# Performance work log

Measured on AMD Instinct MI355X. Metric: run time of the kernel, lower is better.

The kernel has to match this reference:

```python
import jax, jax.numpy as jnp
import numpy as np

B, S, D = 8, 2048, 512


def setup_inputs() -> dict:
    key = jax.random.key(0)
    ks = jax.random.split(key, 11)
    scale = 1.0 / np.sqrt(D)
    inp = {"x": jax.random.normal(ks[0], (B, S, D), dtype=jnp.float32)}
    names = ["q", "k", "v", "g", "o"]
    for i, n in enumerate(names):
        inp[f"W{n}"] = jax.random.normal(ks[1 + 2 * i], (D, D), dtype=jnp.float32) * scale
        inp[f"b{n}"] = jax.random.normal(ks[2 + 2 * i], (D,), dtype=jnp.float32) * 0.01
    return inp


def reference(x, Wq, bq, Wk, bk, Wv, bv, Wg, bg, Wo, bo):
    # Projections (torch nn.Linear: x @ W.T + b)
    Q = x @ Wq.T + bq            # (B,S,D)
    K = x @ Wk.T + bk
    V = x @ Wv.T + bv
    gamma = jax.nn.sigmoid(x @ Wg.T + bg)

    # Recurrent linear-attention scan over time.
    # State St: (B,D,D); update: St = gamma_t[:, :, None] * St + k_t ⊗ v_t
    # (decay broadcasts along the key/row dimension, matching
    #  gamma_i.transpose(1,2) * S in the torch code)
    def step(St, qkvg):
        q_t, k_t, v_t, g_t = qkvg           # each (B,D)
        St = g_t[:, :, None] * St + k_t[:, :, None] * v_t[:, None, :]
        out_t = jnp.einsum('bd,bde->be', q_t, St)  # q_i @ S
        return St, out_t

    S0 = jnp.zeros((B, D, D), dtype=x.dtype)
    # time-major inputs for scan: (S,B,D)
    seq = (Q.transpose(1, 0, 2), K.transpose(1, 0, 2),
           V.transpose(1, 0, 2), gamma.transpose(1, 0, 2))
    _, outs = jax.lax.scan(step, S0, seq)   # outs: (S,B,D)
    O = outs.transpose(1, 0, 2)             # (B,S,D)
    return O @ Wo.T + bo
```

## Files before the change

### kernel.cpp

```cpp
#include <hip/hip_runtime.h>
#include <hip/hip_bf16.h>
#include <stdint.h>


#define B_ 8
#define S_ 2048
#define D_ 512
#define M_ (B_ * S_)
#define NSUB 64
#define SUBL 32
#define NSUP 8
#define SUPL 256

typedef __bf16 bf16x8 __attribute__((ext_vector_type(8)));
typedef float f32x4 __attribute__((ext_vector_type(4)));

__device__ __forceinline__ float bflo(uint32_t u){ return __uint_as_float(u<<16); }
__device__ __forceinline__ float bfhi(uint32_t u){ return __uint_as_float(u&0xffff0000u); }
__device__ __forceinline__ uint16_t f2bf(float f){
    uint32_t u = __float_as_uint(f);
    return (uint16_t)((u + 0x7fffu + ((u>>16)&1u)) >> 16);
}
__device__ __forceinline__ uint32_t pack2bf(float a, float b){
    return (uint32_t)f2bf(a) | ((uint32_t)f2bf(b)<<16);
}
__device__ __forceinline__ void gload16(const void* g, void* l){
    __builtin_amdgcn_global_load_lds(
        (const __attribute__((address_space(1))) uint32_t*)g,
        (__attribute__((address_space(3))) uint32_t*)l, 16, 0, 0);
}

__global__ __launch_bounds__(256) void conv_x(const float* __restrict__ in,
                                              uint16_t* __restrict__ out){
    const size_t i = ((size_t)blockIdx.x*256 + threadIdx.x)*8;
    float4 a = *(const float4*)&in[i];
    float4 b = *(const float4*)&in[i+4];
    uint4 o; o.x=pack2bf(a.x,a.y); o.y=pack2bf(a.z,a.w); o.z=pack2bf(b.x,b.y); o.w=pack2bf(b.z,b.w);
    *(uint4*)&out[i] = o;
}
__global__ __launch_bounds__(256) void conv_w(const float* w0, const float* w1, const float* w2,
                                              const float* w3, const float* w4,
                                              uint16_t* __restrict__ out){
    const float* ws[5] = {w0,w1,w2,w3,w4};
    const float* in = ws[blockIdx.y];
    uint16_t* o = out + (size_t)blockIdx.y*D_*D_;
    const size_t i = ((size_t)blockIdx.x*256 + threadIdx.x)*8;
    float4 a = *(const float4*)&in[i];
    float4 b = *(const float4*)&in[i+4];
    uint4 u; u.x=pack2bf(a.x,a.y); u.y=pack2bf(a.z,a.w); u.z=pack2bf(b.x,b.y); u.w=pack2bf(b.z,b.w);
    *(uint4*)&o[i] = u;
}

__global__ __launch_bounds__(256) void proj4(const uint16_t* __restrict__ A,
                                             const uint16_t* __restrict__ Wb,
                                             const float* __restrict__ bq_,
                                             const float* __restrict__ bk_,
                                             const float* __restrict__ bv_,
                                             const float* __restrict__ bg_,
                                             uint16_t* __restrict__ Qb,
                                             uint16_t* __restrict__ Kb,
                                             uint16_t* __restrict__ VT,
                                             float* __restrict__ Gf)
{
    __shared__ __attribute__((aligned(16))) uint16_t As[128*64];
    __shared__ __attribute__((aligned(16))) uint16_t Bs[128*64];
    const int tid = threadIdx.x, wave = tid>>6, lane = tid&63;
    const int m0 = blockIdx.x*128, n0 = blockIdx.y*128;
    const int wr = (wave>>1)*64, wc = (wave&1)*64;
    const int fr = lane&15, fq = lane>>4;
    f32x4 acc[4][4] = {};

    for (int k0 = 0; k0 < D_; k0 += 64) {
        __syncthreads();
#pragma unroll
        for (int i = 0; i < 4; ++i) {
            const int c = i*256 + tid;
            const int row = c>>3, kc = (c&7)*8;
            const int ldsb = (i*256 + wave*64)*8;
            gload16(&A [(size_t)(m0+row)*D_ + k0 + kc], &As[ldsb]);
            gload16(&Wb[(size_t)(n0+row)*D_ + k0 + kc], &Bs[ldsb]);
        }
        __syncthreads();
#pragma unroll
        for (int kk = 0; kk < 64; kk += 32) {
            bf16x8 af[4], bf[4];
#pragma unroll
            for (int m = 0; m < 4; ++m) af[m] = *(const bf16x8*)&As[(wr+m*16+fr)*64 + kk + fq*8];
#pragma unroll
            for (int n = 0; n < 4; ++n) bf[n] = *(const bf16x8*)&Bs[(wc+n*16+fr)*64 + kk + fq*8];
#pragma unroll
            for (int m = 0; m < 4; ++m)
#pragma unroll
                for (int n = 0; n < 4; ++n)
                    acc[m][n] = __builtin_amdgcn_mfma_f32_16x16x32_bf16(af[m], bf[n], acc[m][n], 0,0,0);
        }
    }
    const int sect = blockIdx.y >> 2;
    const float* bias = (sect==0) ? bq_ : (sect==1) ? bk_ : (sect==2) ? bv_ : bg_;
#pragma unroll
    for (int n = 0; n < 4; ++n) {
        const int coll = (n0 & 511) + wc + n*16 + fr;
        const float bv = bias[coll];
        if (sect == 2) {
#pragma unroll
            for (int m = 0; m < 4; ++m) {
                const int rg = m0 + wr + m*16 + fq*4;
                const int bb = rg >> 11, t = rg & 2047;
                uint2 pk;
                pk.x = pack2bf(acc[m][n][0]+bv, acc[m][n][1]+bv);
                pk.y = pack2bf(acc[m][n][2]+bv, acc[m][n][3]+bv);
                *(uint2*)&VT[((size_t)bb*D_ + coll)*S_ + t] = pk;
            }
        } else if (sect == 3) {
#pragma unroll
            for (int m = 0; m < 4; ++m)
#pragma unroll
                for (int q = 0; q < 4; ++q) {
                    const int row = m0 + wr + m*16 + fq*4 + q;
                    Gf[(size_t)row*D_ + coll] = 1.f/(1.f+expf(-(acc[m][n][q]+bv)));
                }
        } else {
            uint16_t* dst = sect ? Kb : Qb;
#pragma unroll
            for (int m = 0; m < 4; ++m)
#pragma unroll
                for (int q = 0; q < 4; ++q) {
                    const int row = m0 + wr + m*16 + fq*4 + q;
                    dst[(size_t)row*D_ + coll] = f2bf(acc[m][n][q]+bv);
                }
        }
    }
}

__global__ __launch_bounds__(256) void mfma_gemm(const uint16_t* __restrict__ A,
                                                 const uint16_t* __restrict__ Wt,
                                                 const float* __restrict__ bias,
                                                 float* __restrict__ out)
{
    __shared__ __attribute__((aligned(16))) uint16_t As[128*64];
    __shared__ __attribute__((aligned(16))) uint16_t Bs[128*64];
    const int tid = threadIdx.x, wave = tid>>6, lane = tid&63;
    const int m0 = blockIdx.x*128, n0 = blockIdx.y*128;
    const int wr = (wave>>1)*64, wc = (wave&1)*64;
    const int fr = lane&15, fq = lane>>4;
    f32x4 acc[4][4] = {};

    for (int k0 = 0; k0 < D_; k0 += 64) {
        __syncthreads();
#pragma unroll
        for (int i = 0; i < 4; ++i) {
            const int c = i*256 + tid;
            const int row = c>>3, kc = (c&7)*8;
            const int ldsb = (i*256 + wave*64)*8;
            gload16(&A [(size_t)(m0+row)*D_ + k0 + kc], &As[ldsb]);
            gload16(&Wt[(size_t)(n0+row)*D_ + k0 + kc], &Bs[ldsb]);
        }
        __syncthreads();
#pragma unroll
        for (int kk = 0; kk < 64; kk += 32) {
            bf16x8 af[4], bf[4];
#pragma unroll
            for (int m = 0; m < 4; ++m) af[m] = *(const bf16x8*)&As[(wr+m*16+fr)*64 + kk + fq*8];
#pragma unroll
            for (int n = 0; n < 4; ++n) bf[n] = *(const bf16x8*)&Bs[(wc+n*16+fr)*64 + kk + fq*8];
#pragma unroll
            for (int m = 0; m < 4; ++m)
#pragma unroll
                for (int n = 0; n < 4; ++n)
                    acc[m][n] = __builtin_amdgcn_mfma_f32_16x16x32_bf16(af[m], bf[n], acc[m][n], 0,0,0);
        }
    }
#pragma unroll
    for (int n = 0; n < 4; ++n) {
        const int col = n0 + wc + n*16 + fr;
        const float bv = bias[col];
#pragma unroll
        for (int m = 0; m < 4; ++m)
#pragma unroll
            for (int q = 0; q < 4; ++q) {
                const int row = m0 + wr + m*16 + fq*4 + q;
                out[(size_t)row*D_ + col] = acc[m][n][q] + bv;
            }
    }
}

__global__ __launch_bounds__(256) void prep(const float* __restrict__ Gf,
                                            uint16_t* __restrict__ Qb,
                                            uint16_t* __restrict__ Kb,
                                            uint16_t* __restrict__ KT,
                                            float* __restrict__ T)
{
    const int sub = blockIdx.x, b = blockIdx.y;
    const int tid = threadIdx.x;
    const int dk0 = tid*2;
    const size_t rowbase = ((size_t)b*S_ + sub*SUBL)*D_;
    const float*    gp = Gf + rowbase + dk0;
    uint16_t*       qp = Qb + rowbase + dk0;
    uint16_t*       kp = Kb + rowbase + dk0;

    float mu0 = 1.f, mu1 = 1.f;
    uint32_t ksave[SUBL];
#pragma unroll
    for (int t = 0; t < SUBL; ++t) {
        const float2   g  = *(const float2*)(gp + (size_t)t*D_);
        const uint32_t qu = *(const uint32_t*)(qp + (size_t)t*D_);
        const uint32_t ku = *(const uint32_t*)(kp + (size_t)t*D_);
        mu0 = fmaxf(mu0*g.x, 1e-30f);
        mu1 = fmaxf(mu1*g.y, 1e-30f);
        const float r0 = __builtin_amdgcn_rcpf(mu0);
        const float r1 = __builtin_amdgcn_rcpf(mu1);
        *(uint32_t*)(qp + (size_t)t*D_) = pack2bf(bflo(qu)*mu0, bfhi(qu)*mu1);
        const uint32_t kw = pack2bf(bflo(ku)*r0, bfhi(ku)*r1);
        *(uint32_t*)(kp + (size_t)t*D_) = kw;
        ksave[t] = kw;
    }
    T[((size_t)b*NSUB + sub)*D_ + dk0]     = mu0;
    T[((size_t)b*NSUB + sub)*D_ + dk0 + 1] = mu1;

    uint16_t* d0 = &KT[((size_t)b*D_ + dk0)*S_ + sub*SUBL];
    uint16_t* d1 = d0 + S_;
#pragma unroll
    for (int q4 = 0; q4 < 4; ++q4) {
        uint4 lo, hi;
        lo.x = (ksave[q4*8+0]&0xffffu) | (ksave[q4*8+1]<<16);
        lo.y = (ksave[q4*8+2]&0xffffu) | (ksave[q4*8+3]<<16);
        lo.z = (ksave[q4*8+4]&0xffffu) | (ksave[q4*8+5]<<16);
        lo.w = (ksave[q4*8+6]&0xffffu) | (ksave[q4*8+7]<<16);
        hi.x = (ksave[q4*8+0]>>16) | (ksave[q4*8+1]&0xffff0000u);
        hi.y = (ksave[q4*8+2]>>16) | (ksave[q4*8+3]&0xffff0000u);
        hi.z = (ksave[q4*8+4]>>16) | (ksave[q4*8+5]&0xffff0000u);
        hi.w = (ksave[q4*8+6]>>16) | (ksave[q4*8+7]&0xffff0000u);
        *(uint4*)&d0[q4*8] = lo;
        *(uint4*)&d1[q4*8] = hi;
    }
}

__global__ __launch_bounds__(512) void tables(const float* __restrict__ T,
                                              float* __restrict__ Pre,
                                              float* __restrict__ Suf,
                                              float* __restrict__ Lam)
{
    const int b = blockIdx.x, dk = threadIdx.x;
    for (int sp = 0; sp < NSUP; ++sp) {
        float run = 1.f;
#pragma unroll
        for (int m = 0; m < 8; ++m) {
            Pre[((size_t)b*NSUB + sp*8+m)*D_ + dk] = run;
            run *= T[((size_t)b*NSUB + sp*8+m)*D_ + dk];
        }
        Lam[((size_t)b*NSUP + sp)*D_ + dk] = run;
        float rs = 1.f;
#pragma unroll
        for (int m = 7; m >= 0; --m) {
            rs *= T[((size_t)b*NSUB + sp*8+m)*D_ + dk];
            Suf[((size_t)b*NSUB + sp*8+m)*D_ + dk] = rs;
        }
    }
}

__device__ __forceinline__ int swz(int r, int c){ return r*D_ + (c ^ ((r&7)<<3)); }

__global__ __launch_bounds__(256) void pairsA(const uint16_t* __restrict__ Qt,
                                              const uint16_t* __restrict__ Kh,
                                              const float* __restrict__ T,
                                              uint16_t* __restrict__ P)
{
    __shared__ __attribute__((aligned(16))) uint16_t qs[SUBL*D_];
    __shared__ __attribute__((aligned(16))) uint16_t ks[SUBL*D_];
    __shared__ float D_lds[D_];
    const int bx = blockIdx.x, sp = blockIdx.y, b = blockIdx.z;
    const int tid = threadIdx.x, wave = tid>>6, lane = tid&63;
    const int fr = lane&15, fq = lane>>4;
    const int mq = wave>>1, nq = wave&1;
    const int dkA = tid*2, dkB = tid*2+1;

    for (int ii = 0; ii < 2; ++ii) {
        const int i = ii ? 7-bx : bx;
        const size_t qrow = (size_t)b*S_ + sp*SUPL + i*SUBL;
        const size_t prow = ((size_t)(b*NSUP + sp)*SUPL + i*SUBL);

#pragma unroll
        for (int z = 0; z < 8; ++z) {
            int ch = z*256 + tid, r = ch>>6, c = (ch&63)*8;
            *(uint4*)&qs[swz(r,c)] = *(const uint4*)&Qt[(qrow + r)*D_ + c];
            *(uint4*)&ks[swz(r,c)] = *(const uint4*)&Kh[(qrow + r)*D_ + c];
        }
        float d0 = 1.f, d1 = 1.f;

        for (int j = i; j >= 0; --j) {
            if (j < i) {
                d0 *= T[((size_t)b*NSUB + sp*8 + j)*D_ + dkA];
                d1 *= T[((size_t)b*NSUB + sp*8 + j)*D_ + dkB];
                D_lds[dkA] = d0; D_lds[dkB] = d1;
                __syncthreads();
#pragma unroll
                for (int z = 0; z < 8; ++z) {
                    int ch = z*256 + tid, r = ch>>6, c = (ch&63)*8;
                    uint4 u = *(const uint4*)&Kh[((size_t)b*S_ + sp*SUPL + j*SUBL + r)*D_ + c];
                    uint4 o;
                    o.x = pack2bf(bflo(u.x)*D_lds[c+0], bfhi(u.x)*D_lds[c+1]);
                    o.y = pack2bf(bflo(u.y)*D_lds[c+2], bfhi(u.y)*D_lds[c+3]);
                    o.z = pack2bf(bflo(u.z)*D_lds[c+4], bfhi(u.z)*D_lds[c+5]);
                    o.w = pack2bf(bflo(u.w)*D_lds[c+6], bfhi(u.w)*D_lds[c+7]);
                    *(uint4*)&ks[swz(r,c)] = o;
                }
            }
            __syncthreads();
            f32x4 a0 = {}, a1 = {}, a2 = {}, a3 = {};
#pragma unroll
            for (int kk = 0; kk < 512; kk += 128) {
                bf16x8 q0 = *(const bf16x8*)&qs[swz(mq*16+fr, kk      + fq*8)];
                bf16x8 k0 = *(const bf16x8*)&ks[swz(nq*16+fr, kk      + fq*8)];
                bf16x8 q1 = *(const bf16x8*)&qs[swz(mq*16+fr, kk + 32 + fq*8)];
                bf16x8 k1 = *(const bf16x8*)&ks[swz(nq*16+fr, kk + 32 + fq*8)];
                bf16x8 q2 = *(const bf16x8*)&qs[swz(mq*16+fr, kk + 64 + fq*8)];
                bf16x8 k2 = *(const bf16x8*)&ks[swz(nq*16+fr, kk + 64 + fq*8)];
                bf16x8 q3 = *(const bf16x8*)&qs[swz(mq*16+fr, kk + 96 + fq*8)];
                bf16x8 k3 = *(const bf16x8*)&ks[swz(nq*16+fr, kk + 96 + fq*8)];
                a0 = __builtin_amdgcn_mfma_f32_16x16x32_bf16(q0, k0, a0, 0,0,0);
                a1 = __builtin_amdgcn_mfma_f32_16x16x32_bf16(q1, k1, a1, 0,0,0);
                a2 = __builtin_amdgcn_mfma_f32_16x16x32_bf16(q2, k2, a2, 0,0,0);
                a3 = __builtin_amdgcn_mfma_f32_16x16x32_bf16(q3, k3, a3, 0,0,0);
            }
            const int ul = nq*16 + fr;
#pragma unroll
            for (int q_ = 0; q_ < 4; ++q_) {
                const int tl = mq*16 + fq*4 + q_;
                float v = a0[q_] + a1[q_] + a2[q_] + a3[q_];
                if (j == i && ul > tl) v = 0.f;
                P[(prow + tl)*SUPL + j*SUBL + ul] = f2bf(v);
            }
            __syncthreads();
        }
    }
}

__global__ __launch_bounds__(256) void dsgemm(const uint16_t* __restrict__ VT,
                                              const uint16_t* __restrict__ KT,
                                              const float* __restrict__ Suf,
                                              uint16_t* __restrict__ Sst)
{
    __shared__ __attribute__((aligned(16))) uint16_t As[128][40];
    __shared__ __attribute__((aligned(16))) uint16_t Bs[128][40];
    const int tile = blockIdx.x, c = blockIdx.y, b = blockIdx.z;
    const int m0 = (tile&3)*128, n0 = (tile>>2)*128;
    const int tid = threadIdx.x, wave = tid>>6, lane = tid&63;
    const int wr = (wave>>1)*64, wc = (wave&1)*64;
    const int fr = lane&15, fq = lane>>4;
    f32x4 acc[4][4] = {};

    for (int j = 0; j < 8; ++j) {
        const int t0 = c*SUPL + j*SUBL;
        __syncthreads();
#pragma unroll
        for (int ch = tid; ch < 512; ch += 256) {
            int row = ch>>2, tc = (ch&3)*8;
            *(uint4*)&As[row][tc] = *(const uint4*)&VT[((size_t)b*D_ + m0+row)*S_ + t0 + tc];
        }
#pragma unroll
        for (int ch = tid; ch < 512; ch += 256) {
            int row = ch>>2, tc = (ch&3)*8;
            uint4 u = *(const uint4*)&KT[((size_t)b*D_ + n0+row)*S_ + t0 + tc];
            float sf = Suf[((size_t)b*NSUB + c*8 + j)*D_ + n0 + row];
            uint4 o;
            o.x = pack2bf(bflo(u.x)*sf, bfhi(u.x)*sf);
            o.y = pack2bf(bflo(u.y)*sf, bfhi(u.y)*sf);
            o.z = pack2bf(bflo(u.z)*sf, bfhi(u.z)*sf);
            o.w = pack2bf(bflo(u.w)*sf, bfhi(u.w)*sf);
            *(uint4*)&Bs[row][tc] = o;
        }
        __syncthreads();
        bf16x8 af[4], bf[4];
#pragma unroll
        for (int m = 0; m < 4; ++m) af[m] = *(const bf16x8*)&As[wr+m*16+fr][fq*8];
#pragma unroll
        for (int n = 0; n < 4; ++n) bf[n] = *(const bf16x8*)&Bs[wc+n*16+fr][fq*8];
#pragma unroll
        for (int m = 0; m < 4; ++m)
#pragma unroll
            for (int n = 0; n < 4; ++n)
                acc[m][n] = __builtin_amdgcn_mfma_f32_16x16x32_bf16(af[m], bf[n], acc[m][n], 0,0,0);
    }
#pragma unroll
    for (int n = 0; n < 4; ++n) {
        const int dk = n0 + wc + n*16 + fr;
#pragma unroll
        for (int m = 0; m < 4; ++m)
#pragma unroll
            for (int q = 0; q < 4; ++q) {
                const int dv = m0 + wr + m*16 + fq*4 + q;
                Sst[(((size_t)c*B_ + b)*D_ + dv)*D_ + dk] = f2bf(acc[m][n][q]);
            }
    }
}

__global__ __launch_bounds__(256) void scanfix(uint16_t* __restrict__ Sst,
                                               const float* __restrict__ Lam)
{
    const int id = blockIdx.x*256 + threadIdx.x;
    const int g = id & 63, dv = (id>>6) & 511, b = id >> 15;
    const int dk = g*8;
    float s[8];
    {
        uint4 u = *(const uint4*)&Sst[(((size_t)0*B_ + b)*D_ + dv)*D_ + dk];
        s[0]=bflo(u.x); s[1]=bfhi(u.x); s[2]=bflo(u.y); s[3]=bfhi(u.y);
        s[4]=bflo(u.z); s[5]=bfhi(u.z); s[6]=bflo(u.w); s[7]=bfhi(u.w);
    }
    for (int c = 1; c < 7; ++c) {
        const size_t bs = (((size_t)c*B_ + b)*D_ + dv)*D_ + dk;
        uint4 d = *(const uint4*)&Sst[bs];
        float4 l0 = *(const float4*)&Lam[((size_t)b*NSUP + c)*D_ + dk];
        float4 l1 = *(const float4*)&Lam[((size_t)b*NSUP + c)*D_ + dk + 4];
        s[0] = l0.x*s[0] + bflo(d.x); s[1] = l0.y*s[1] + bfhi(d.x);
        s[2] = l0.z*s[2] + bflo(d.y); s[3] = l0.w*s[3] + bfhi(d.y);
        s[4] = l1.x*s[4] + bflo(d.z); s[5] = l1.y*s[5] + bfhi(d.z);
        s[6] = l1.z*s[6] + bflo(d.w); s[7] = l1.w*s[7] + bfhi(d.w);
        uint4 o;
        o.x = pack2bf(s[0],s[1]); o.y = pack2bf(s[2],s[3]);
        o.z = pack2bf(s[4],s[5]); o.w = pack2bf(s[6],s[7]);
        *(uint4*)&Sst[bs] = o;
    }
}

__global__ __launch_bounds__(256) void bigout(const uint16_t* __restrict__ Qt,
                                              const float* __restrict__ Pre,
                                              const uint16_t* __restrict__ Sst,
                                              const uint16_t* __restrict__ Pb,
                                              const uint16_t* __restrict__ VT,
                                              uint16_t* __restrict__ O)
{
    __shared__ __attribute__((aligned(16))) uint16_t As[128*64];
    __shared__ __attribute__((aligned(16))) uint16_t Bs[128*64];
    __shared__ float PreL[4*512];
    const int m0 = blockIdx.x*128, n0 = blockIdx.y*128;
    const int b = blockIdx.z>>3, sp = blockIdx.z&7;
    const int tid = threadIdx.x, wave = tid>>6, lane = tid&63;
    const int wr = (wave>>1)*64, wc = (wave&1)*64;
    const int fr = lane&15, fq = lane>>4;
    const int i0 = m0>>5;

#pragma unroll
    for (int z = 0; z < 8; ++z) {
        int idx = z*256 + tid;
        PreL[idx] = Pre[((size_t)b*NSUB + sp*8 + i0 + (idx>>9))*D_ + (idx&511)];
    }
    f32x4 acc[4][4] = {};
    const int kt0 = (sp == 0) ? 8 : 0;
    for (int kt = kt0; kt < 12; ++kt) {
        __syncthreads();
        if (kt < 8) {
            const int k0 = kt*64;
#pragma unroll
            for (int z = 0; z < 4; ++z) {
                int ch = z*256 + tid, r = ch>>3, cc = (ch&7)*8;
                uint4 u = *(const uint4*)&Qt[((size_t)b*S_ + sp*SUPL + m0 + r)*D_ + k0 + cc];
                const float* pr = &PreL[((r>>5)<<9) + k0 + cc];
                uint4 o;
                o.x = pack2bf(bflo(u.x)*pr[0], bfhi(u.x)*pr[1]);
                o.y = pack2bf(bflo(u.y)*pr[2], bfhi(u.y)*pr[3]);
                o.z = pack2bf(bflo(u.z)*pr[4], bfhi(u.z)*pr[5]);
                o.w = pack2bf(bflo(u.w)*pr[6], bfhi(u.w)*pr[7]);
                *(uint4*)&As[r*64 + cc] = o;
            }
#pragma unroll
            for (int z = 0; z < 4; ++z) {
                int ch = z*256 + tid, row = ch>>3, cc = (ch&7)*8;
                int ldsb = (z*256 + wave*64)*8;
                gload16(&Sst[(((size_t)(sp-1)*B_ + b)*D_ + n0 + row)*D_ + k0 + cc], &Bs[ldsb]);
            }
        } else {
            const int u0 = (kt-8)*64;
#pragma unroll
            for (int z = 0; z < 4; ++z) {
                int ch = z*256 + tid, row = ch>>3, cc = (ch&7)*8;
                int ldsb = (z*256 + wave*64)*8;
                gload16(&Pb[((size_t)(b*NSUP + sp)*SUPL + m0 + row)*SUPL + u0 + cc], &As[ldsb]);
                gload16(&VT[((size_t)b*D_ + n0 + row)*S_ + sp*SUPL + u0 + cc], &Bs[ldsb]);
            }
        }
        __syncthreads();
#pragma unroll
        for (int kk = 0; kk < 64; kk += 32) {
            bf16x8 af[4], bf[4];
#pragma unroll
            for (int m = 0; m < 4; ++m) af[m] = *(const bf16x8*)&As[(wr+m*16+fr)*64 + kk + fq*8];
#pragma unroll
            for (int n = 0; n < 4; ++n) bf[n] = *(const bf16x8*)&Bs[(wc+n*16+fr)*64 + kk + fq*8];
#pragma unroll
            for (int m = 0; m < 4; ++m)
#pragma unroll
                for (int n = 0; n < 4; ++n)
                    acc[m][n] = __builtin_amdgcn_mfma_f32_16x16x32_bf16(af[m], bf[n], acc[m][n], 0,0,0);
        }
    }
#pragma unroll
    for (int n = 0; n < 4; ++n) {
        const int dv = n0 + wc + n*16 + fr;
#pragma unroll
        for (int m = 0; m < 4; ++m)
#pragma unroll
            for (int q = 0; q < 4; ++q) {
                const int t = sp*SUPL + m0 + wr + m*16 + fq*4 + q;
                O[((size_t)b*S_ + t)*D_ + dv] = f2bf(acc[m][n][q]);
            }
    }
}

extern "C" void kernel_launch(void* const* d_in, const int* in_sizes, int n_in,
                              void* d_out, int out_size, void* d_ws, size_t ws_size,
                              hipStream_t stream)
{
    (void)in_sizes; (void)n_in; (void)out_size; (void)ws_size;
    const float* x  = (const float*)d_in[0];
    const float* Wq = (const float*)d_in[1];  const float* bq = (const float*)d_in[2];
    const float* Wk = (const float*)d_in[3];  const float* bk = (const float*)d_in[4];
    const float* Wv = (const float*)d_in[5];  const float* bv = (const float*)d_in[6];
    const float* Wg = (const float*)d_in[7];  const float* bg = (const float*)d_in[8];
    const float* Wo = (const float*)d_in[9];  const float* bo = (const float*)d_in[10];

    char* w = (char*)d_ws;
    const size_t MD2 = (size_t)M_*D_*2;
    uint16_t* Wb = (uint16_t*)w;                       w += 5*(size_t)D_*D_*2;
    uint16_t* xb = (uint16_t*)w;                       w += MD2;
    uint16_t* Qb = (uint16_t*)w;                       w += MD2;
    uint16_t* Kb = (uint16_t*)w;                       w += MD2;
    uint16_t* KT = (uint16_t*)w;                       w += MD2;
    uint16_t* VT = (uint16_t*)w;                       w += MD2;
    float*    Gf = (float*)w;                          w += (size_t)M_*D_*4;
    uint16_t* Sst = (uint16_t*)w;                      w += (size_t)7*B_*D_*D_*2;
    uint16_t* Pb  = (uint16_t*)w;                      w += (size_t)B_*NSUP*SUPL*SUPL*2;
    float*    T   = (float*)w;                         w += (size_t)B_*NSUB*D_*4;
    float*    Pre = (float*)w;                         w += (size_t)B_*NSUB*D_*4;
    float*    Suf = (float*)w;                         w += (size_t)B_*NSUB*D_*4;
    float*    Lam = (float*)w;                         w += (size_t)B_*NSUP*D_*4;

    hipMemsetAsync(Pb, 0, (size_t)B_*NSUP*SUPL*SUPL*2, stream);

    conv_x<<<dim3(M_*D_/2048), 256, 0, stream>>>(x, xb);
    conv_w<<<dim3(D_*D_/2048, 5), 256, 0, stream>>>(Wq, Wk, Wv, Wg, Wo, Wb);

    proj4<<<dim3(M_/128, 16), 256, 0, stream>>>(xb, Wb, bq, bk, bv, bg, Qb, Kb, VT, Gf);

    prep<<<dim3(NSUB, B_), 256, 0, stream>>>(Gf, Qb, Kb, KT, T);
    tables<<<dim3(B_), 512, 0, stream>>>(T, Pre, Suf, Lam);

    pairsA<<<dim3(4, NSUP, B_), 256, 0, stream>>>(Qb, Kb, T, Pb);
    dsgemm<<<dim3(16, 7, B_), 256, 0, stream>>>(VT, KT, Suf, Sst);
    scanfix<<<dim3(1024), 256, 0, stream>>>(Sst, Lam);

    bigout<<<dim3(2, 4, B_*NSUP), 256, 0, stream>>>(Qb, Pre, Sst, Pb, VT, xb);

    mfma_gemm<<<dim3(M_/128, D_/128), 256, 0, stream>>>(xb, Wb + 4*(size_t)D_*D_, bo, (float*)d_out);
}
```

Baseline: 236.1 us.

## Swizzle LDS tiles and stage GEMM epilogues through shared memory for coalesced stores

Applies an XOR swizzle to the 64-wide bf16 LDS tiles in the projection, output and chunk GEMMs so MFMA fragment reads avoid bank conflicts. Epilogues now write accumulator tiles into a padded shared buffer and then emit 16-byte coalesced global stores for Q/K/G/output/O. The V transpose is produced by swapping MFMA operand order and going through LDS. The change adds extra barriers and a shared-memory round trip per tile.

Measured after the change: 218.1 us. 1.08x faster.

```diff
diff --git a/kernel.cpp b/kernel.cpp
--- a/kernel.cpp
+++ b/kernel.cpp
@@ -62,8 +62,124 @@
                                              uint16_t* __restrict__ VT,
                                              float* __restrict__ Gf)
 {
-    __shared__ __attribute__((aligned(16))) uint16_t As[128*64];
-    __shared__ __attribute__((aligned(16))) uint16_t Bs[128*64];
+    __shared__ __attribute__((aligned(16))) uint16_t SM[17472];
+    uint16_t* As = SM;
+    uint16_t* Bs = SM + 8192;
+    const int tid = threadIdx.x, wave = tid>>6, lane = tid&63;
+    const int m0 = blockIdx.x*128, n0 = blockIdx.y*128;
+    const int wr = (wave>>1)*64, wc = (wave&1)*64;
+    const int fr = lane&15, fq = lane>>4;
+    const int sect = blockIdx.y >> 2;
+    const int n0c = n0 & 511;
+    f32x4 acc[4][4] = {};
+
+    for (int k0 = 0; k0 < D_; k0 += 64) {
+        __syncthreads();
+#pragma unroll
+        for (int i = 0; i < 4; ++i) {
+            const int c = i*256 + tid;
+            const int row = c>>3, kc = ((c&7) ^ (row&7))*8;
+            const int ldsb = (i*256 + wave*64)*8;
+            gload16(&A [(size_t)(m0+row)*D_ + k0 + kc], &As[ldsb]);
+            gload16(&Wb[(size_t)(n0+row)*D_ + k0 + kc], &Bs[ldsb]);
+        }
+        __syncthreads();
+#pragma unroll
+        for (int kk = 0; kk < 64; kk += 32) {
+            const int sc = (kk + fq*8) ^ ((fr&7)<<3);
+            bf16x8 af[4], bf[4];
+#pragma unroll
+            for (int m = 0; m < 4; ++m) af[m] = *(const bf16x8*)&As[(wr+m*16+fr)*64 + sc];
+#pragma unroll
+            for (int n = 0; n < 4; ++n) bf[n] = *(const bf16x8*)&Bs[(wc+n*16+fr)*64 + sc];
+            if (sect == 2) {
+#pragma unroll
+                for (int m = 0; m < 4; ++m)
+#pragma unroll
+                    for (int n = 0; n < 4; ++n)
+                        acc[m][n] = __builtin_amdgcn_mfma_f32_16x16x32_bf16(bf[n], af[m], acc[m][n], 0,0,0);
+            } else {
+#pragma unroll
+                for (int m = 0; m < 4; ++m)
+#pragma unroll
+                    for (int n = 0; n < 4; ++n)
+                        acc[m][n] = __builtin_amdgcn_mfma_f32_16x16x32_bf16(af[m], bf[n], acc[m][n], 0,0,0);
+            }
+        }
+    }
+    __syncthreads();
+
+    if (sect == 3) {
+        float (*L32)[68] = (float(*)[68])SM;
+#pragma unroll
+        for (int h = 0; h < 2; ++h) {
+            if (wc == h*64) {
+#pragma unroll
+                for (int n = 0; n < 4; ++n) {
+                    const float bvv = bg_[n0c + wc + n*16 + fr];
+#pragma unroll
+                    for (int m = 0; m < 4; ++m)
+#pragma unroll
+                        for (int q = 0; q < 4; ++q)
+                            L32[wr + m*16 + fq*4 + q][n*16 + fr] =
+                                1.f/(1.f + expf(-(acc[m][n][q] + bvv)));
+                }
+            }
+            __syncthreads();
+#pragma unroll
+            for (int it = 0; it < 8; ++it) {
+                const int r = it*16 + (tid>>4), c4 = (tid&15)*4;
+                *(uint4*)&Gf[(size_t)(m0+r)*D_ + n0c + h*64 + c4] = *(uint4*)&L32[r][c4];
+            }
+            __syncthreads();
+        }
+    } else {
+        uint16_t (*L)[136] = (uint16_t(*)[136])SM;
+        const float* bias = (sect==0) ? bq_ : (sect==1) ? bk_ : bv_;
+        if (sect == 2) {
+#pragma unroll
+            for (int n = 0; n < 4; ++n)
+#pragma unroll
+                for (int q = 0; q < 4; ++q) {
+                    const int dvl = wc + n*16 + fq*4 + q;
+                    const float bvv = bias[n0c + dvl];
+#pragma unroll
+                    for (int m = 0; m < 4; ++m)
+                        L[dvl][wr + m*16 + fr] = f2bf(acc[m][n][q] + bvv);
+                }
+        } else {
+#pragma unroll
+            for (int n = 0; n < 4; ++n) {
+                const int cl = wc + n*16 + fr;
+                const float bvv = bias[n0c + cl];
+#pragma unroll
+                for (int m = 0; m < 4; ++m)
+#pragma unroll
+                    for (int q = 0; q < 4; ++q)
+                        L[wr + m*16 + fq*4 + q][cl] = f2bf(acc[m][n][q] + bvv);
+            }
+        }
+        __syncthreads();
+        const int bb = m0 >> 11, t0 = m0 & 2047;
+#pragma unroll
+        for (int it = 0; it < 8; ++it) {
+            const int r = it*16 + (tid>>4), c8 = (tid&15)*8;
+            uint4 v = *(uint4*)&L[r][c8];
+            if (sect == 0)      *(uint4*)&Qb[(size_t)(m0+r)*D_ + n0c + c8] = v;
+            else if (sect == 1) *(uint4*)&Kb[(size_t)(m0+r)*D_ + n0c + c8] = v;
+            else                *(uint4*)&VT[((size_t)bb*D_ + n0c + r)*S_ + t0 + c8] = v;
+        }
+    }
+}
+
+__global__ __launch_bounds__(256) void mfma_gemm(const uint16_t* __restrict__ A,
+                                                 const uint16_t* __restrict__ Wt,
+                                                 const float* __restrict__ bias,
+                                                 float* __restrict__ out)
+{
+    __shared__ __attribute__((aligned(16))) uint16_t SM[17472];
+    uint16_t* As = SM;
+    uint16_t* Bs = SM + 8192;
     const int tid = threadIdx.x, wave = tid>>6, lane = tid&63;
     const int m0 = blockIdx.x*128, n0 = blockIdx.y*128;
     const int wr = (wave>>1)*64, wc = (wave&1)*64;
@@ -75,82 +191,7 @@
 #pragma unroll
         for (int i = 0; i < 4; ++i) {
             const int c = i*256 + tid;
-            const int row = c>>3, kc = (c&7)*8;
-            const int ldsb = (i*256 + wave*64)*8;
-            gload16(&A [(size_t)(m0+row)*D_ + k0 + kc], &As[ldsb]);
-            gload16(&Wb[(size_t)(n0+row)*D_ + k0 + kc], &Bs[ldsb]);
-        }
-        __syncthreads();
-#pragma unroll
-        for (int kk = 0; kk < 64; kk += 32) {
-            bf16x8 af[4], bf[4];
-#pragma unroll
-            for (int m = 0; m < 4; ++m) af[m] = *(const bf16x8*)&As[(wr+m*16+fr)*64 + kk + fq*8];
-#pragma unroll
-            for (int n = 0; n < 4; ++n) bf[n] = *(const bf16x8*)&Bs[(wc+n*16+fr)*64 + kk + fq*8];
-#pragma unroll
-            for (int m = 0; m < 4; ++m)
-#pragma unroll
-                for (int n = 0; n < 4; ++n)
-                    acc[m][n] = __builtin_amdgcn_mfma_f32_16x16x32_bf16(af[m], bf[n], acc[m][n], 0,0,0);
-        }
-    }
-    const int sect = blockIdx.y >> 2;
-    const float* bias = (sect==0) ? bq_ : (sect==1) ? bk_ : (sect==2) ? bv_ : bg_;
-#pragma unroll
-    for (int n = 0; n < 4; ++n) {
-        const int coll = (n0 & 511) + wc + n*16 + fr;
-        const float bv = bias[coll];
-        if (sect == 2) {
-#pragma unroll
-            for (int m = 0; m < 4; ++m) {
-                const int rg = m0 + wr + m*16 + fq*4;
-                const int bb = rg >> 11, t = rg & 2047;
-                uint2 pk;
-                pk.x = pack2bf(acc[m][n][0]+bv, acc[m][n][1]+bv);
-                pk.y = pack2bf(acc[m][n][2]+bv, acc[m][n][3]+bv);
-                *(uint2*)&VT[((size_t)bb*D_ + coll)*S_ + t] = pk;
-            }
-        } else if (sect == 3) {
-#pragma unroll
-            for (int m = 0; m < 4; ++m)
-#pragma unroll
-                for (int q = 0; q < 4; ++q) {
-                    const int row = m0 + wr + m*16 + fq*4 + q;
-                    Gf[(size_t)row*D_ + coll] = 1.f/(1.f+expf(-(acc[m][n][q]+bv)));
-                }
-        } else {
-            uint16_t* dst = sect ? Kb : Qb;
-#pragma unroll
-            for (int m = 0; m < 4; ++m)
-#pragma unroll
-                for (int q = 0; q < 4; ++q) {
-                    const int row = m0 + wr + m*16 + fq*4 + q;
-                    dst[(size_t)row*D_ + coll] = f2bf(acc[m][n][q]+bv);
-                }
-        }
-    }
-}
-
-__global__ __launch_bounds__(256) void mfma_gemm(const uint16_t* __restrict__ A,
-                                                 const uint16_t* __restrict__ Wt,
-                                                 const float* __restrict__ bias,
-                                                 float* __restrict__ out)
-{
-    __shared__ __attribute__((aligned(16))) uint16_t As[128*64];
-    __shared__ __attribute__((aligned(16))) uint16_t Bs[128*64];
-    const int tid = threadIdx.x, wave = tid>>6, lane = tid&63;
-    const int m0 = blockIdx.x*128, n0 = blockIdx.y*128;
-    const int wr = (wave>>1)*64, wc = (wave&1)*64;
-    const int fr = lane&15, fq = lane>>4;
-    f32x4 acc[4][4] = {};
-
-    for (int k0 = 0; k0 < D_; k0 += 64) {
-        __syncthreads();
-#pragma unroll
-        for (int i = 0; i < 4; ++i) {
-            const int c = i*256 + tid;
-            const int row = c>>3, kc = (c&7)*8;
+            const int row = c>>3, kc = ((c&7) ^ (row&7))*8;
             const int ldsb = (i*256 + wave*64)*8;
             gload16(&A [(size_t)(m0+row)*D_ + k0 + kc], &As[ldsb]);
             gload16(&Wt[(size_t)(n0+row)*D_ + k0 + kc], &Bs[ldsb]);
@@ -158,11 +199,12 @@
         __syncthreads();
 #pragma unroll
         for (int kk = 0; kk < 64; kk += 32) {
+            const int sc = (kk + fq*8) ^ ((fr&7)<<3);
             bf16x8 af[4], bf[4];
 #pragma unroll
-            for (int m = 0; m < 4; ++m) af[m] = *(const bf16x8*)&As[(wr+m*16+fr)*64 + kk + fq*8];
-#pragma unroll
-            for (int n = 0; n < 4; ++n) bf[n] = *(const bf16x8*)&Bs[(wc+n*16+fr)*64 + kk + fq*8];
+            for (int m = 0; m < 4; ++m) af[m] = *(const bf16x8*)&As[(wr+m*16+fr)*64 + sc];
+#pragma unroll
+            for (int n = 0; n < 4; ++n) bf[n] = *(const bf16x8*)&Bs[(wc+n*16+fr)*64 + sc];
 #pragma unroll
             for (int m = 0; m < 4; ++m)
 #pragma unroll
@@ -170,17 +212,28 @@
                     acc[m][n] = __builtin_amdgcn_mfma_f32_16x16x32_bf16(af[m], bf[n], acc[m][n], 0,0,0);
         }
     }
-#pragma unroll
-    for (int n = 0; n < 4; ++n) {
-        const int col = n0 + wc + n*16 + fr;
-        const float bv = bias[col];
-#pragma unroll
-        for (int m = 0; m < 4; ++m)
-#pragma unroll
-            for (int q = 0; q < 4; ++q) {
-                const int row = m0 + wr + m*16 + fq*4 + q;
-                out[(size_t)row*D_ + col] = acc[m][n][q] + bv;
-            }
+    __syncthreads();
+    float (*L32)[68] = (float(*)[68])SM;
+#pragma unroll
+    for (int h = 0; h < 2; ++h) {
+        if (wc == h*64) {
+#pragma unroll
+            for (int n = 0; n < 4; ++n) {
+                const float bvv = bias[n0 + wc + n*16 + fr];
+#pragma unroll
+                for (int m = 0; m < 4; ++m)
+#pragma unroll
+                    for (int q = 0; q < 4; ++q)
+                        L32[wr + m*16 + fq*4 + q][n*16 + fr] = acc[m][n][q] + bvv;
+            }
+        }
+        __syncthreads();
+#pragma unroll
+        for (int it = 0; it < 8; ++it) {
+            const int r = it*16 + (tid>>4), c4 = (tid&15)*4;
+            *(uint4*)&out[(size_t)(m0+r)*D_ + n0 + h*64 + c4] = *(uint4*)&L32[r][c4];
+        }
+        __syncthreads();
     }
 }
 
@@ -429,9 +482,10 @@
                                               const uint16_t* __restrict__ VT,
                                               uint16_t* __restrict__ O)
 {
-    __shared__ __attribute__((aligned(16))) uint16_t As[128*64];
-    __shared__ __attribute__((aligned(16))) uint16_t Bs[128*64];
+    __shared__ __attribute__((aligned(16))) uint16_t SM[17472];
     __shared__ float PreL[4*512];
+    uint16_t* As = SM;
+    uint16_t* Bs = SM + 8192;
     const int m0 = blockIdx.x*128, n0 = blockIdx.y*128;
     const int b = blockIdx.z>>3, sp = blockIdx.z&7;
     const int tid = threadIdx.x, wave = tid>>6, lane = tid&63;
@@ -460,32 +514,33 @@
                 o.y = pack2bf(bflo(u.y)*pr[2], bfhi(u.y)*pr[3]);
                 o.z = pack2bf(bflo(u.z)*pr[4], bfhi(u.z)*pr[5]);
                 o.w = pack2bf(bflo(u.w)*pr[6], bfhi(u.w)*pr[7]);
-                *(uint4*)&As[r*64 + cc] = o;
+                *(uint4*)&As[r*64 + (cc ^ ((r&7)<<3))] = o;
             }
 #pragma unroll
             for (int z = 0; z < 4; ++z) {
-                int ch = z*256 + tid, row = ch>>3, cc = (ch&7)*8;
+                int ch = z*256 + tid, row = ch>>3, kc = ((ch&7) ^ (row&7))*8;
                 int ldsb = (z*256 + wave*64)*8;
-                gload16(&Sst[(((size_t)(sp-1)*B_ + b)*D_ + n0 + row)*D_ + k0 + cc], &Bs[ldsb]);
+                gload16(&Sst[(((size_t)(sp-1)*B_ + b)*D_ + n0 + row)*D_ + k0 + kc], &Bs[ldsb]);
             }
         } else {
             const int u0 = (kt-8)*64;
 #pragma unroll
             for (int z = 0; z < 4; ++z) {
-                int ch = z*256 + tid, row = ch>>3, cc = (ch&7)*8;
+                int ch = z*256 + tid, row = ch>>3, kc = ((ch&7) ^ (row&7))*8;
                 int ldsb = (z*256 + wave*64)*8;
-                gload16(&Pb[((size_t)(b*NSUP + sp)*SUPL + m0 + row)*SUPL + u0 + cc], &As[ldsb]);
-                gload16(&VT[((size_t)b*D_ + n0 + row)*S_ + sp*SUPL + u0 + cc], &Bs[ldsb]);
+                gload16(&Pb[((size_t)(b*NSUP + sp)*SUPL + m0 + row)*SUPL + u0 + kc], &As[ldsb]);
+                gload16(&VT[((size_t)b*D_ + n0 + row)*S_ + sp*SUPL + u0 + kc], &Bs[ldsb]);
             }
         }
         __syncthreads();
 #pragma unroll
         for (int kk = 0; kk < 64; kk += 32) {
+            const int sc = (kk + fq*8) ^ ((fr&7)<<3);
             bf16x8 af[4], bf[4];
 #pragma unroll
-            for (int m = 0; m < 4; ++m) af[m] = *(const bf16x8*)&As[(wr+m*16+fr)*64 + kk + fq*8];
-#pragma unroll
-            for (int n = 0; n < 4; ++n) bf[n] = *(const bf16x8*)&Bs[(wc+n*16+fr)*64 + kk + fq*8];
+            for (int m = 0; m < 4; ++m) af[m] = *(const bf16x8*)&As[(wr+m*16+fr)*64 + sc];
+#pragma unroll
+            for (int n = 0; n < 4; ++n) bf[n] = *(const bf16x8*)&Bs[(wc+n*16+fr)*64 + sc];
 #pragma unroll
             for (int m = 0; m < 4; ++m)
 #pragma unroll
@@ -493,16 +548,22 @@
                     acc[m][n] = __builtin_amdgcn_mfma_f32_16x16x32_bf16(af[m], bf[n], acc[m][n], 0,0,0);
         }
     }
+    __syncthreads();
+    uint16_t (*L)[136] = (uint16_t(*)[136])SM;
 #pragma unroll
     for (int n = 0; n < 4; ++n) {
-        const int dv = n0 + wc + n*16 + fr;
+        const int cl = wc + n*16 + fr;
 #pragma unroll
         for (int m = 0; m < 4; ++m)
 #pragma unroll
-            for (int q = 0; q < 4; ++q) {
-                const int t = sp*SUPL + m0 + wr + m*16 + fq*4 + q;
-                O[((size_t)b*S_ + t)*D_ + dv] = f2bf(acc[m][n][q]);
-            }
+            for (int q = 0; q < 4; ++q)
+                L[wr + m*16 + fq*4 + q][cl] = f2bf(acc[m][n][q]);
+    }
+    __syncthreads();
+#pragma unroll
+    for (int it = 0; it < 8; ++it) {
+        const int r = it*16 + (tid>>4), c8 = (tid&15)*8;
+        *(uint4*)&O[((size_t)b*S_ + sp*SUPL + m0 + r)*D_ + n0 + c8] = *(uint4*)&L[r][c8];
     }
 }
 
```
